# Kernel optimization log

Measured on AMD Instinct MI355X. Metric: run time of the kernel, lower is better.

The kernel has to match this reference:

```python
import jax, jax.numpy as jnp
import numpy as np

D = 1024
H = 16
HS = 64

def setup_inputs() -> dict:
    key = jax.random.key(0)
    ks = jax.random.split(key, 9)
    s = 0.02
    x = jax.random.normal(ks[0], (2, 4096, D), dtype=jnp.float32)
    Wq = jax.random.normal(ks[1], (H, D, HS), dtype=jnp.float32) * s
    Wk = jax.random.normal(ks[2], (H, D, HS), dtype=jnp.float32) * s
    Wv = jax.random.normal(ks[3], (H, D, HS), dtype=jnp.float32) * s
    bq = jax.random.normal(ks[4], (H, HS), dtype=jnp.float32) * s
    bk = jax.random.normal(ks[5], (H, HS), dtype=jnp.float32) * s
    bv = jax.random.normal(ks[6], (H, HS), dtype=jnp.float32) * s
    Wp = jax.random.normal(ks[7], (D, D), dtype=jnp.float32) * s
    bp = jax.random.normal(ks[8], (D,), dtype=jnp.float32) * s
    return {"x": x, "Wq": Wq, "Wk": Wk, "Wv": Wv, "bq": bq, "bk": bk, "bv": bv, "Wp": Wp, "bp": bp}

def reference(x, Wq, Wk, Wv, bq, bk, bv, Wp, bp):
    B, T, _ = x.shape
    # per-head projections, stacked over heads: [B, H, T, HS]
    q = jnp.einsum('btd,hde->bhte', x, Wq) + bq[None, :, None, :]
    k = jnp.einsum('btd,hde->bhte', x, Wk) + bk[None, :, None, :]
    v = jnp.einsum('btd,hde->bhte', x, Wv) + bv[None, :, None, :]
    scale = 1.0 / jnp.sqrt(jnp.float32(HS))
    scores = jnp.einsum('bhte,bhse->bhts', q, k) * scale  # [B,H,T,T]
    causal = jnp.tril(jnp.ones((T, T), dtype=bool))
    scores = jnp.where(causal[None, None, :, :], scores, -jnp.inf)
    attn = jax.nn.softmax(scores, axis=-1)
    out = jnp.einsum('bhts,bhse->bhte', attn, v)  # [B,H,T,HS]
    # concat heads along last dim (head order preserved)
    out = out.transpose(0, 2, 1, 3).reshape(B, T, H * HS)
    return out @ Wp + bp
```

## Files before the change

kernel.cpp:

```cpp
#include <hip/hip_runtime.h>
#include <hip/hip_bf16.h>
#include <stdint.h>


typedef __bf16 bf16x8 __attribute__((ext_vector_type(8)));
typedef float f32x4 __attribute__((ext_vector_type(4)));
typedef float f32x16 __attribute__((ext_vector_type(16)));
typedef __attribute__((address_space(1))) void gvoid_t;
typedef __attribute__((address_space(3))) void lvoid_t;

using hbf = __hip_bfloat16;

#define QSCALE (0.125f * 1.44269504088896f)

static __device__ __forceinline__ void gload_lds16(const void* g, void* l) {
  __builtin_amdgcn_global_load_lds((gvoid_t*)g, (lvoid_t*)l, 16, 0, 0);
}

static __device__ __forceinline__ uint16_t b2u(float x) {
  hbf h = __float2bfloat16(x);
  return *reinterpret_cast<uint16_t*>(&h);
}

static __device__ __forceinline__ uint32_t cvtpk(float lo, float hi) {
  uint32_t r;
  asm("v_cvt_pk_bf16_f32 %0, %1, %2" : "=v"(r) : "v"(lo), "v"(hi));
  return r;
}

static __device__ __forceinline__ void pl32swap(uint32_t& x, uint32_t& y) {
  asm volatile("v_permlane32_swap_b32 %0, %1" : "+v"(x), "+v"(y));
}

static __device__ __forceinline__ float max3f(float a, float b, float c) {
  return fmaxf(fmaxf(a, b), c);
}


__global__ void k_cvt_all(const float* __restrict__ x,
                          const float* __restrict__ Wq, const float* __restrict__ Wk,
                          const float* __restrict__ Wv,
                          const float* __restrict__ bq, const float* __restrict__ bk,
                          const float* __restrict__ bv,
                          const float* __restrict__ Wp,
                          hbf* __restrict__ xb, hbf* __restrict__ Wt,
                          hbf* __restrict__ Wpt, float* __restrict__ biasc) {
  const int b = blockIdx.x, tid = threadIdx.x;
  if (b < 8192) {
    int i = (b * 256 + tid) * 4;
    float4 v = *reinterpret_cast<const float4*>(x + i);
    hbf h[4] = {__float2bfloat16(v.x), __float2bfloat16(v.y),
                __float2bfloat16(v.z), __float2bfloat16(v.w)};
    *reinterpret_cast<ushort4*>(xb + i) = *reinterpret_cast<ushort4*>(h);
  } else if (b < 20480) {
    int idx = (b - 8192) * 256 + tid;
    int d = idx & 1023, r = idx >> 10;
    int m = r >> 10, rem = r & 1023;
    int h = rem >> 6, e = rem & 63;
    const float* W = (m == 0) ? Wq : (m == 1) ? Wk : Wv;
    float v = W[(h << 10 | d) * 64 + e];
    if (m == 0) v *= QSCALE;
    Wt[idx] = __float2bfloat16(v);
  } else if (b < 24576) {
    int idx = (b - 20480) * 256 + tid;
    int o = idx >> 10, d = idx & 1023;
    Wpt[idx] = __float2bfloat16(Wp[(d << 10) + o]);
  } else {
    int r = (b - 24576) * 256 + tid;
    int m = r >> 10, rem = r & 1023;
    const float* bsrc = (m == 0) ? bq : (m == 1) ? bk : bv;
    float v = bsrc[rem];
    if (m == 0) v *= QSCALE;
    biasc[r] = v;
  }
}


__global__ __launch_bounds__(512) void k_gemm_qkv(
    const hbf* __restrict__ A, const hbf* __restrict__ Bw,
    const float* __restrict__ biasc, hbf* __restrict__ qkv) {
  __shared__ __align__(16) hbf sA[2][128 * 64];
  __shared__ __align__(16) hbf sB[2][256 * 64];
  const int tid = threadIdx.x;
  const int lane = tid & 63, w = tid >> 6;
  const int wm = w >> 2, wn = w & 3;
  const int g = lane >> 4, cl = lane & 15;
  const int m0 = blockIdx.x * 128, n0 = blockIdx.y * 256;

  const int sr = tid >> 3, sc = tid & 7;

  const f32x4 fz = {0.f, 0.f, 0.f, 0.f};
  f32x4 acc[4][4];
#pragma unroll
  for (int a = 0; a < 4; ++a)
#pragma unroll
    for (int b = 0; b < 4; ++b) acc[a][b] = fz;

#pragma unroll
  for (int kt = 0; kt < 2; ++kt) {
#pragma unroll
    for (int s = 0; s < 2; ++s) {
      const int row = s * 64 + sr;
      gload_lds16(A + (size_t)(m0 + row) * 1024 + kt * 64 + ((sc ^ (row & 7)) * 8),
                  &sA[kt][s * 4096 + tid * 8]);
    }
#pragma unroll
    for (int s = 0; s < 4; ++s) {
      const int row = s * 64 + sr;
      gload_lds16(Bw + (size_t)(n0 + row) * 1024 + kt * 64 + ((sc ^ (row & 7)) * 8),
                  &sB[kt][s * 4096 + tid * 8]);
    }
  }
  asm volatile("s_waitcnt vmcnt(6)" ::: "memory");
  __builtin_amdgcn_s_barrier();

  for (int kt = 0; kt < 16; ++kt) {
    const int bi = kt & 1;
    const bool st = (kt + 2) < 16;

    bf16x8 af[4][2], bf[4][2];
#pragma unroll
    for (int rt = 0; rt < 4; ++rt)
#pragma unroll
      for (int ks = 0; ks < 2; ++ks)
        af[rt][ks] = *reinterpret_cast<const bf16x8*>(
            &sA[bi][(wm * 64 + rt * 16 + cl) * 64 + (((ks * 4 + g) ^ (cl & 7)) * 8)]);
#pragma unroll
    for (int ct = 0; ct < 4; ++ct)
#pragma unroll
      for (int ks = 0; ks < 2; ++ks)
        bf[ct][ks] = *reinterpret_cast<const bf16x8*>(
            &sB[bi][(wn * 64 + ct * 16 + cl) * 64 + (((ks * 4 + g) ^ (cl & 7)) * 8)]);
    __builtin_amdgcn_s_barrier();
    asm volatile("s_waitcnt lgkmcnt(0)" ::: "memory");
    __builtin_amdgcn_sched_barrier(0);
    __builtin_amdgcn_s_setprio(1);
#pragma unroll
    for (int rt = 0; rt < 4; ++rt)
#pragma unroll
      for (int ks = 0; ks < 2; ++ks)
        acc[rt][0] = __builtin_amdgcn_mfma_f32_16x16x32_bf16(af[rt][ks], bf[0][ks], acc[rt][0], 0, 0, 0);
    __builtin_amdgcn_s_setprio(0);
    __builtin_amdgcn_s_barrier();

#pragma unroll
    for (int q = 1; q < 4; ++q) {
      if (st) {
        if (q == 1) {
#pragma unroll
          for (int s = 0; s < 2; ++s) {
            const int row = s * 64 + sr;
            gload_lds16(A + (size_t)(m0 + row) * 1024 + (kt + 2) * 64 + ((sc ^ (row & 7)) * 8),
                        &sA[bi][s * 4096 + tid * 8]);
          }
        } else {
#pragma unroll
          for (int s2 = 0; s2 < 2; ++s2) {
            const int s = (q - 2) * 2 + s2;
            const int row = s * 64 + sr;
            gload_lds16(Bw + (size_t)(n0 + row) * 1024 + (kt + 2) * 64 + ((sc ^ (row & 7)) * 8),
                        &sB[bi][s * 4096 + tid * 8]);
          }
        }
      }
      __builtin_amdgcn_s_setprio(1);
#pragma unroll
      for (int rt = 0; rt < 4; ++rt)
#pragma unroll
        for (int ks = 0; ks < 2; ++ks)
          acc[rt][q] = __builtin_amdgcn_mfma_f32_16x16x32_bf16(af[rt][ks], bf[q][ks], acc[rt][q], 0, 0, 0);
      __builtin_amdgcn_s_setprio(0);
      if (q == 3) {
        if (st) asm volatile("s_waitcnt vmcnt(6)" ::: "memory");
        else    asm volatile("s_waitcnt vmcnt(0)" ::: "memory");
      }
      __builtin_amdgcn_s_barrier();
    }
  }

#pragma unroll
  for (int rt = 0; rt < 4; ++rt)
#pragma unroll
    for (int ct = 0; ct < 4; ++ct) {
      const int colg = n0 + wn * 64 + ct * 16 + cl;
      const int mi = colg >> 10, rem = colg & 1023;
      const int h = rem >> 6, e = rem & 63;
      const float bi_ = biasc[colg];
      if (mi == 2) {
        const int t0 = m0 + wm * 64 + rt * 16 + g * 4;
        const int b = t0 >> 12, t = t0 & 4095;
        ushort4 o;
        o.x = b2u(acc[rt][ct][0] + bi_);
        o.y = b2u(acc[rt][ct][1] + bi_);
        o.z = b2u(acc[rt][ct][2] + bi_);
        o.w = b2u(acc[rt][ct][3] + bi_);
        *reinterpret_cast<ushort4*>(
            qkv + (size_t)64 * 262144 + (size_t)(b * 16 + h) * 262144 + (size_t)e * 4096 + t) = o;
      } else {
#pragma unroll
        for (int i = 0; i < 4; ++i) {
          const int rowg = m0 + wm * 64 + rt * 16 + g * 4 + i;
          const int b = rowg >> 12, t = rowg & 4095;
          qkv[(((size_t)mi * 32 + b * 16 + h) * 4096 + t) * 64 + e] =
              __float2bfloat16(acc[rt][ct][i] + bi_);
        }
      }
    }
}


__global__ __launch_bounds__(256) void k_flash(
    const hbf* __restrict__ qkv, hbf* __restrict__ attn) {
  __shared__ __align__(16) __bf16 sK[2][64 * 64];
  __shared__ __align__(16) __bf16 sV[2][64 * 64];
  const int tid = threadIdx.x, lane = tid & 63, wq = tid >> 6;
  const int h = lane >> 5, r31 = lane & 31;
  const int bh = blockIdx.x;
  const int qtb = (int)gridDim.y - 1 - (int)blockIdx.y;
  const int q0 = qtb * 128;
  const int ntile = 2 * qtb + 2;
  const hbf* Q  = qkv + (size_t)bh * 262144;
  const hbf* Kp = qkv + (size_t)(32 + bh) * 262144;
  const hbf* Vp = qkv + (size_t)(64 + bh) * 262144;
  const float NEG_INF = -__builtin_inff();

  const int koff = (wq * 16 + (lane >> 3)) * 64 + (((lane & 7) ^ (lane >> 3)) * 8);
  const int voff = (wq * 16 + (lane >> 3)) * 4096 + (((lane & 7) ^ (lane >> 3)) * 8);

  const int qrow = q0 + wq * 32 + r31;
  bf16x8 aq[4];
#pragma unroll
  for (int ks = 0; ks < 4; ++ks)
    aq[ks] = *reinterpret_cast<const bf16x8*>(Q + (size_t)qrow * 64 + ks * 16 + h * 8);

  f32x16 accO[2];
#pragma unroll
  for (int et = 0; et < 2; ++et)
#pragma unroll
    for (int i = 0; i < 16; ++i) accO[et][i] = 0.f;
  float mrow = NEG_INF, lrow = 0.f;

  gload_lds16(Kp + koff,         &sK[0][wq * 1024]);
  gload_lds16(Kp + koff + 512,   &sK[0][wq * 1024 + 512]);
  gload_lds16(Vp + voff,         &sV[0][wq * 1024]);
  gload_lds16(Vp + voff + 32768, &sV[0][wq * 1024 + 512]);
  __syncthreads();

  const int qmaxw = q0 + wq * 32 + 31;
  int buf = 0;
  for (int jt = 0; jt < ntile; ++jt) {
    if (jt < ntile - 1) {
      const hbf* Kg = Kp + (size_t)(jt + 1) * 4096;
      gload_lds16(Kg + koff,       &sK[buf ^ 1][wq * 1024]);
      gload_lds16(Kg + koff + 512, &sK[buf ^ 1][wq * 1024 + 512]);
      const hbf* Vg = Vp + (jt + 1) * 64;
      gload_lds16(Vg + voff,         &sV[buf ^ 1][wq * 1024]);
      gload_lds16(Vg + voff + 32768, &sV[buf ^ 1][wq * 1024 + 512]);
    }

    if (64 * jt <= qmaxw) {
      const __bf16* sKb = sK[buf];
      const __bf16* sVb = sV[buf];

      f32x16 accS[2];
      __builtin_amdgcn_s_setprio(1);
#pragma unroll
      for (int t = 0; t < 2; ++t) {
        f32x16 s;
#pragma unroll
        for (int i = 0; i < 16; ++i) s[i] = 0.f;
#pragma unroll
        for (int ks = 0; ks < 4; ++ks) {
          bf16x8 ak = *reinterpret_cast<const bf16x8*>(
              sKb + (t * 32 + r31) * 64 + (((2 * ks + h) ^ (r31 & 7)) * 8));
          s = __builtin_amdgcn_mfma_f32_32x32x16_bf16(ak, aq[ks], s, 0, 0, 0);
        }
        accS[t] = s;
      }
      __builtin_amdgcn_s_setprio(0);

      if (64 * jt + 63 > q0 + wq * 32) {
#pragma unroll
        for (int t = 0; t < 2; ++t)
#pragma unroll
          for (int i = 0; i < 16; ++i) {
            const int kvg = 64 * jt + 32 * t + (i & 3) + 8 * (i >> 2) + 4 * h;
            if (kvg > qrow) accS[t][i] = NEG_INF;
          }
      }

      float g0 = max3f(accS[0][0], accS[0][1], accS[0][2]);
      float g1 = max3f(accS[0][3], accS[0][4], accS[0][5]);
      float g2 = max3f(accS[0][6], accS[0][7], accS[0][8]);
      float g3 = max3f(accS[0][9], accS[0][10], accS[0][11]);
      float g4 = max3f(accS[0][12], accS[0][13], accS[0][14]);
      float g5 = max3f(accS[0][15], accS[1][0], accS[1][1]);
      float g6 = max3f(accS[1][2], accS[1][3], accS[1][4]);
      float g7 = max3f(accS[1][5], accS[1][6], accS[1][7]);
      float g8 = max3f(accS[1][8], accS[1][9], accS[1][10]);
      float g9 = max3f(accS[1][11], accS[1][12], accS[1][13]);
      float gA = fmaxf(accS[1][14], accS[1][15]);
      float h0 = max3f(g0, g1, g2);
      float h1 = max3f(g3, g4, g5);
      float h2 = max3f(g6, g7, g8);
      float h3 = fmaxf(g9, gA);
      float pmax = fmaxf(max3f(h0, h1, h2), h3);
      pmax = fmaxf(pmax, __shfl_xor(pmax, 32));

      if (!__all(pmax - mrow <= 8.f)) {
        const float mn = fmaxf(mrow, pmax);
        const float corr = __builtin_amdgcn_exp2f(mrow - mn);
        mrow = mn;
        lrow *= corr;
#pragma unroll
        for (int et = 0; et < 2; ++et)
#pragma unroll
          for (int i = 0; i < 16; ++i) accO[et][i] *= corr;
      }

#pragma unroll
      for (int t = 0; t < 2; ++t)
#pragma unroll
        for (int i = 0; i < 16; ++i)
          accS[t][i] = __builtin_amdgcn_exp2f(accS[t][i] - mrow);
      float s0 = (accS[0][0] + accS[0][1]) + (accS[0][2] + accS[0][3]);
      float s1 = (accS[0][4] + accS[0][5]) + (accS[0][6] + accS[0][7]);
      float s2 = (accS[0][8] + accS[0][9]) + (accS[0][10] + accS[0][11]);
      float s3 = (accS[0][12] + accS[0][13]) + (accS[0][14] + accS[0][15]);
      float s4 = (accS[1][0] + accS[1][1]) + (accS[1][2] + accS[1][3]);
      float s5 = (accS[1][4] + accS[1][5]) + (accS[1][6] + accS[1][7]);
      float s6 = (accS[1][8] + accS[1][9]) + (accS[1][10] + accS[1][11]);
      float s7 = (accS[1][12] + accS[1][13]) + (accS[1][14] + accS[1][15]);
      float rs = ((s0 + s1) + (s2 + s3)) + ((s4 + s5) + (s6 + s7));
      rs += __shfl_xor(rs, 32);
      lrow += rs;

      uint32_t d0[2][4], d1[2][4];
#pragma unroll
      for (int t = 0; t < 2; ++t)
#pragma unroll
        for (int r4 = 0; r4 < 4; ++r4) {
          d0[t][r4] = cvtpk(accS[t][4 * r4 + 0], accS[t][4 * r4 + 1]);
          d1[t][r4] = cvtpk(accS[t][4 * r4 + 2], accS[t][4 * r4 + 3]);
        }

#pragma unroll
      for (int kb = 0; kb < 4; ++kb) {
        const int t = kb >> 1, ra = 2 * (kb & 1), rb = ra + 1;
        uint32_t x0 = d0[t][ra], y0 = d0[t][rb];
        uint32_t x1 = d1[t][ra], y1 = d1[t][rb];
        pl32swap(x0, y0);
        pl32swap(x1, y1);
        union { uint32_t u[4]; bf16x8 v; } bP;
        bP.u[0] = x0; bP.u[1] = x1; bP.u[2] = y0; bP.u[3] = y1;
        __builtin_amdgcn_s_setprio(1);
#pragma unroll
        for (int et = 0; et < 2; ++et) {
          bf16x8 av = *reinterpret_cast<const bf16x8*>(
              sVb + (et * 32 + r31) * 64 + (((2 * kb + h) ^ (r31 & 7)) * 8));
          accO[et] = __builtin_amdgcn_mfma_f32_32x32x16_bf16(av, bP.v, accO[et], 0, 0, 0);
        }
        __builtin_amdgcn_s_setprio(0);
      }
    }

    __syncthreads();
    buf ^= 1;
  }

  const float inv = 1.0f / lrow;
  hbf* arow = attn + ((size_t)(bh >> 4) * 4096 + qrow) * 1024 + (bh & 15) * 64;
#pragma unroll
  for (int et = 0; et < 2; ++et)
#pragma unroll
    for (int r4 = 0; r4 < 4; ++r4) {
      const int e0 = et * 32 + 8 * r4 + 4 * h;
      ushort4 o;
      o.x = b2u(accO[et][4 * r4 + 0] * inv);
      o.y = b2u(accO[et][4 * r4 + 1] * inv);
      o.z = b2u(accO[et][4 * r4 + 2] * inv);
      o.w = b2u(accO[et][4 * r4 + 3] * inv);
      *reinterpret_cast<ushort4*>(arow + e0) = o;
    }
}


__global__ __launch_bounds__(256) void k_gemm_out(
    const hbf* __restrict__ A, const hbf* __restrict__ Bw,
    const float* __restrict__ bp, float* __restrict__ out) {
  __shared__ __align__(16) hbf sA[128 * 64];
  __shared__ __align__(16) hbf sB[128 * 64];
  const int tid = threadIdx.x;
  const int lane = tid & 63, wid = tid >> 6;
  const int m0 = blockIdx.x * 128, n0 = blockIdx.y * 128;
  const int g = lane >> 4, cl = lane & 15;

  const f32x4 fz = {0.f, 0.f, 0.f, 0.f};
  f32x4 acc[4][4];
#pragma unroll
  for (int a = 0; a < 4; ++a)
#pragma unroll
    for (int b = 0; b < 4; ++b) acc[a][b] = fz;

  const int srow = wid * 32 + (lane >> 3);
  const int scol = (lane & 7) * 8;

  for (int kt = 0; kt < 16; ++kt) {
    const int k0 = kt * 64;
#pragma unroll
    for (int t = 0; t < 4; ++t) {
      const int r = srow + t * 8;
      gload_lds16(A + (size_t)(m0 + r) * 1024 + k0 + scol, sA + (wid * 32 + t * 8) * 64);
      gload_lds16(Bw + (size_t)(n0 + r) * 1024 + k0 + scol, sB + (wid * 32 + t * 8) * 64);
    }
    __syncthreads();
#pragma unroll
    for (int ks = 0; ks < 2; ++ks) {
      const int ko = ks * 32 + g * 8;
      bf16x8 af[4], bfr[4];
#pragma unroll
      for (int rt = 0; rt < 4; ++rt)
        af[rt] = *reinterpret_cast<const bf16x8*>(sA + ((wid & 1) * 64 + rt * 16 + cl) * 64 + ko);
#pragma unroll
      for (int ct = 0; ct < 4; ++ct)
        bfr[ct] = *reinterpret_cast<const bf16x8*>(sB + ((wid >> 1) * 64 + ct * 16 + cl) * 64 + ko);
#pragma unroll
      for (int rt = 0; rt < 4; ++rt)
#pragma unroll
        for (int ct = 0; ct < 4; ++ct)
          acc[rt][ct] = __builtin_amdgcn_mfma_f32_16x16x32_bf16(af[rt], bfr[ct], acc[rt][ct], 0, 0, 0);
    }
    __syncthreads();
  }

#pragma unroll
  for (int rt = 0; rt < 4; ++rt)
#pragma unroll
    for (int ct = 0; ct < 4; ++ct) {
      const int colg = n0 + (wid >> 1) * 64 + ct * 16 + cl;
      const float bi = bp[colg];
#pragma unroll
      for (int i = 0; i < 4; ++i) {
        const int rowg = m0 + (wid & 1) * 64 + rt * 16 + g * 4 + i;
        out[(size_t)rowg * 1024 + colg] = acc[rt][ct][i] + bi;
      }
    }
}


extern "C" void kernel_launch(void* const* d_in, const int* in_sizes, int n_in,
                              void* d_out, int out_size, void* d_ws, size_t ws_size,
                              hipStream_t stream) {
  const float* x  = (const float*)d_in[0];
  const float* Wq = (const float*)d_in[1];
  const float* Wk = (const float*)d_in[2];
  const float* Wv = (const float*)d_in[3];
  const float* bq = (const float*)d_in[4];
  const float* bk = (const float*)d_in[5];
  const float* bv = (const float*)d_in[6];
  const float* Wp = (const float*)d_in[7];
  const float* bp = (const float*)d_in[8];
  float* out = (float*)d_out;

  char* ws = (char*)d_ws;
  hbf*   xb    = (hbf*)ws;
  hbf*   Wt    = (hbf*)(ws + 16777216);
  hbf*   Wpt   = (hbf*)(ws + 16777216 + 6291456);
  float* biasc = (float*)(ws + 16777216 + 6291456 + 2097152);
  hbf*   qkv   = (hbf*)(ws + 16777216 + 6291456 + 2097152 + 16384);
  hbf*   attn  = xb;

  k_cvt_all<<<24588, 256, 0, stream>>>(x, Wq, Wk, Wv, bq, bk, bv, Wp,
                                       xb, Wt, Wpt, biasc);

  dim3 g1(64, 12); k_gemm_qkv<<<g1, 512, 0, stream>>>(xb, Wt, biasc, qkv);
  dim3 g2(32, 32); k_flash   <<<g2, 256, 0, stream>>>(qkv, attn);
  dim3 g3(64, 8);  k_gemm_out<<<g3, 256, 0, stream>>>(attn, Wpt, bp, out);
}
```

Baseline: 219.0 us.

## Rewrite output projection GEMM with double-buffered swizzled LDS pipeline and larger tiles

The output projection GEMM now mirrors the QKV GEMM design. It uses 512 threads, 128x256 tiles, and double-buffered LDS with XOR-swizzled layout to avoid bank conflicts. Loads for stage k+2 are interleaved between MFMA groups using fine-grained barriers, vmcnt waits and setprio. This is meant to hide global load latency behind compute and cut the per-tile synchronization stalls of the old single-buffer loop. The grid halves to 64x4 blocks, which may reduce occupancy and wave parallelism on the device.

```diff
diff --git a/kernel.cpp b/kernel.cpp
--- a/kernel.cpp
+++ b/kernel.cpp
@@ -86,7 +86,6 @@
   const int wm = w >> 2, wn = w & 3;
   const int g = lane >> 4, cl = lane & 15;
   const int m0 = blockIdx.x * 128, n0 = blockIdx.y * 256;
-
   const int sr = tid >> 3, sc = tid & 7;
 
   const f32x4 fz = {0.f, 0.f, 0.f, 0.f};
@@ -385,15 +384,17 @@
 }
 
 
-__global__ __launch_bounds__(256) void k_gemm_out(
+__global__ __launch_bounds__(512) void k_gemm_out(
     const hbf* __restrict__ A, const hbf* __restrict__ Bw,
     const float* __restrict__ bp, float* __restrict__ out) {
-  __shared__ __align__(16) hbf sA[128 * 64];
-  __shared__ __align__(16) hbf sB[128 * 64];
+  __shared__ __align__(16) hbf sA[2][128 * 64];
+  __shared__ __align__(16) hbf sB[2][256 * 64];
   const int tid = threadIdx.x;
-  const int lane = tid & 63, wid = tid >> 6;
-  const int m0 = blockIdx.x * 128, n0 = blockIdx.y * 128;
+  const int lane = tid & 63, w = tid >> 6;
+  const int wm = w >> 2, wn = w & 3;
   const int g = lane >> 4, cl = lane & 15;
+  const int m0 = blockIdx.x * 128, n0 = blockIdx.y * 256;
+  const int sr = tid >> 3, sc = tid & 7;
 
   const f32x4 fz = {0.f, 0.f, 0.f, 0.f};
   f32x4 acc[4][4];
@@ -402,47 +403,98 @@
 #pragma unroll
     for (int b = 0; b < 4; ++b) acc[a][b] = fz;
 
-  const int srow = wid * 32 + (lane >> 3);
-  const int scol = (lane & 7) * 8;
+#pragma unroll
+  for (int kt = 0; kt < 2; ++kt) {
+#pragma unroll
+    for (int s = 0; s < 2; ++s) {
+      const int row = s * 64 + sr;
+      gload_lds16(A + (size_t)(m0 + row) * 1024 + kt * 64 + ((sc ^ (row & 7)) * 8),
+                  &sA[kt][s * 4096 + tid * 8]);
+    }
+#pragma unroll
+    for (int s = 0; s < 4; ++s) {
+      const int row = s * 64 + sr;
+      gload_lds16(Bw + (size_t)(n0 + row) * 1024 + kt * 64 + ((sc ^ (row & 7)) * 8),
+                  &sB[kt][s * 4096 + tid * 8]);
+    }
+  }
+  asm volatile("s_waitcnt vmcnt(6)" ::: "memory");
+  __builtin_amdgcn_s_barrier();
 
   for (int kt = 0; kt < 16; ++kt) {
-    const int k0 = kt * 64;
-#pragma unroll
-    for (int t = 0; t < 4; ++t) {
-      const int r = srow + t * 8;
-      gload_lds16(A + (size_t)(m0 + r) * 1024 + k0 + scol, sA + (wid * 32 + t * 8) * 64);
-      gload_lds16(Bw + (size_t)(n0 + r) * 1024 + k0 + scol, sB + (wid * 32 + t * 8) * 64);
-    }
-    __syncthreads();
-#pragma unroll
-    for (int ks = 0; ks < 2; ++ks) {
-      const int ko = ks * 32 + g * 8;
-      bf16x8 af[4], bfr[4];
+    const int bi = kt & 1;
+    const bool st = (kt + 2) < 16;
+
+    bf16x8 af[4][2], bf[4][2];
+#pragma unroll
+    for (int rt = 0; rt < 4; ++rt)
+#pragma unroll
+      for (int ks = 0; ks < 2; ++ks)
+        af[rt][ks] = *reinterpret_cast<const bf16x8*>(
+            &sA[bi][(wm * 64 + rt * 16 + cl) * 64 + (((ks * 4 + g) ^ (cl & 7)) * 8)]);
+#pragma unroll
+    for (int ct = 0; ct < 4; ++ct)
+#pragma unroll
+      for (int ks = 0; ks < 2; ++ks)
+        bf[ct][ks] = *reinterpret_cast<const bf16x8*>(
+            &sB[bi][(wn * 64 + ct * 16 + cl) * 64 + (((ks * 4 + g) ^ (cl & 7)) * 8)]);
+    __builtin_amdgcn_s_barrier();
+    asm volatile("s_waitcnt lgkmcnt(0)" ::: "memory");
+    __builtin_amdgcn_sched_barrier(0);
+    __builtin_amdgcn_s_setprio(1);
+#pragma unroll
+    for (int rt = 0; rt < 4; ++rt)
+#pragma unroll
+      for (int ks = 0; ks < 2; ++ks)
+        acc[rt][0] = __builtin_amdgcn_mfma_f32_16x16x32_bf16(af[rt][ks], bf[0][ks], acc[rt][0], 0, 0, 0);
+    __builtin_amdgcn_s_setprio(0);
+    __builtin_amdgcn_s_barrier();
+
+#pragma unroll
+    for (int q = 1; q < 4; ++q) {
+      if (st) {
+        if (q == 1) {
+#pragma unroll
+          for (int s = 0; s < 2; ++s) {
+            const int row = s * 64 + sr;
+            gload_lds16(A + (size_t)(m0 + row) * 1024 + (kt + 2) * 64 + ((sc ^ (row & 7)) * 8),
+                        &sA[bi][s * 4096 + tid * 8]);
+          }
+        } else {
+#pragma unroll
+          for (int s2 = 0; s2 < 2; ++s2) {
+            const int s = (q - 2) * 2 + s2;
+            const int row = s * 64 + sr;
+            gload_lds16(Bw + (size_t)(n0 + row) * 1024 + (kt + 2) * 64 + ((sc ^ (row & 7)) * 8),
+                        &sB[bi][s * 4096 + tid * 8]);
+          }
+        }
+      }
+      __builtin_amdgcn_s_setprio(1);
 #pragma unroll
       for (int rt = 0; rt < 4; ++rt)
-        af[rt] = *reinterpret_cast<const bf16x8*>(sA + ((wid & 1) * 64 + rt * 16 + cl) * 64 + ko);
-#pragma unroll
-      for (int ct = 0; ct < 4; ++ct)
-        bfr[ct] = *reinterpret_cast<const bf16x8*>(sB + ((wid >> 1) * 64 + ct * 16 + cl) * 64 + ko);
-#pragma unroll
-      for (int rt = 0; rt < 4; ++rt)
-#pragma unroll
-        for (int ct = 0; ct < 4; ++ct)
-          acc[rt][ct] = __builtin_amdgcn_mfma_f32_16x16x32_bf16(af[rt], bfr[ct], acc[rt][ct], 0, 0, 0);
-    }
-    __syncthreads();
+#pragma unroll
+        for (int ks = 0; ks < 2; ++ks)
+          acc[rt][q] = __builtin_amdgcn_mfma_f32_16x16x32_bf16(af[rt][ks], bf[q][ks], acc[rt][q], 0, 0, 0);
+      __builtin_amdgcn_s_setprio(0);
+      if (q == 3) {
+        if (st) asm volatile("s_waitcnt vmcnt(6)" ::: "memory");
+        else    asm volatile("s_waitcnt vmcnt(0)" ::: "memory");
+      }
+      __builtin_amdgcn_s_barrier();
+    }
   }
 
 #pragma unroll
   for (int rt = 0; rt < 4; ++rt)
 #pragma unroll
     for (int ct = 0; ct < 4; ++ct) {
-      const int colg = n0 + (wid >> 1) * 64 + ct * 16 + cl;
-      const float bi = bp[colg];
+      const int colg = n0 + wn * 64 + ct * 16 + cl;
+      const float bi_ = bp[colg];
 #pragma unroll
       for (int i = 0; i < 4; ++i) {
-        const int rowg = m0 + (wid & 1) * 64 + rt * 16 + g * 4 + i;
-        out[(size_t)rowg * 1024 + colg] = acc[rt][ct][i] + bi;
+        const int rowg = m0 + wm * 64 + rt * 16 + g * 4 + i;
+        out[(size_t)rowg * 1024 + colg] = acc[rt][ct][i] + bi_;
       }
     }
 }
@@ -475,5 +527,5 @@
 
   dim3 g1(64, 12); k_gemm_qkv<<<g1, 512, 0, stream>>>(xb, Wt, biasc, qkv);
   dim3 g2(32, 32); k_flash   <<<g2, 256, 0, stream>>>(qkv, attn);
-  dim3 g3(64, 8);  k_gemm_out<<<g3, 256, 0, stream>>>(attn, Wpt, bp, out);
-}
+  dim3 g3(64, 4);  k_gemm_out<<<g3, 512, 0, stream>>>(attn, Wpt, bp, out);
+}
```

After: 212.4 us. 3.0% less time.
